# Performance work log

Hardware: AMD Instinct MI355X
Metric: run time of the kernel (lower is better)

Reference implementation:

```python
import jax, jax.numpy as jnp
import numpy as np

DIM = 1024
HEADS = 16
SCALE = DIM ** -0.5  # NOTE: original uses full dim, not head dim


def setup_inputs() -> dict:
    key = jax.random.key(0)
    k1, k2, k3, k4 = jax.random.split(key, 4)
    x = jax.random.normal(k1, (2, 2048, DIM), dtype=jnp.float32)
    # torch nn.Linear(dim, 3*dim, bias=False): y = x @ W_qkv (stored here as [dim, 3*dim])
    w_qkv = jax.random.normal(k2, (DIM, 3 * DIM), dtype=jnp.float32) * (DIM ** -0.5)
    w_out = jax.random.normal(k3, (DIM, DIM), dtype=jnp.float32) * (DIM ** -0.5)
    b_out = jax.random.normal(k4, (DIM,), dtype=jnp.float32) * 0.01
    return {"x": x, "w_qkv": w_qkv, "w_out": w_out, "b_out": b_out}


def reference(x, w_qkv, w_out, b_out):
    b, n, d = x.shape
    h = HEADS
    hd = d // h
    qkv = x @ w_qkv  # [b, n, 3*d]
    # last dim layout is (qkv, h, hd) per rearrange 'b n (qkv h d) -> qkv b h n d'
    qkv = qkv.reshape(b, n, 3, h, hd)
    q, k, v = (jnp.moveaxis(qkv, (2, 3), (0, 2))[i] for i in range(3))  # each [b, h, n, hd]
    dots = jnp.einsum('bhid,bhjd->bhij', q, k) * SCALE
    causal_mask = jnp.triu(jnp.ones((n, n), dtype=bool), k=1)
    dots = jnp.where(causal_mask, -jnp.inf, dots)
    attn = jax.nn.softmax(dots, axis=-1)
    out = jnp.einsum('bhij,bhjd->bhid', attn, v)
    out = jnp.moveaxis(out, 1, 2).reshape(b, n, d)  # 'b h n d -> b n (h d)'
    return out @ w_out + b_out
```

## Files before the change

kernel.cpp:

```cpp
#include <hip/hip_runtime.h>

typedef __attribute__((ext_vector_type(8))) short bf16x8;
typedef __attribute__((ext_vector_type(4))) float f32x4;
typedef unsigned short u16;
typedef unsigned int u32;

#define SEQ 2048
#define NHEAD 16
#define EXP2_SCALE 0.045084219f

__device__ __forceinline__ u16 f2bf(float f){
  u32 u = __builtin_bit_cast(u32, f);
  u += 0x7FFFu + ((u >> 16) & 1u);
  return (u16)(u >> 16);
}

__device__ __forceinline__ void gl16(const u16* g, u16* l){
  __builtin_amdgcn_global_load_lds(
      (__attribute__((address_space(1))) void*)(unsigned long long)(const void*)g,
      (__attribute__((address_space(3))) void*)(unsigned)(unsigned long long)(const void*)l,
      16, 0, 0);
}

__global__ __launch_bounds__(256) void prep(const float* __restrict__ x,
                                            const float* __restrict__ w_qkv,
                                            const float* __restrict__ w_out,
                                            u16* __restrict__ xb,
                                            u16* __restrict__ wqkvT,
                                            u16* __restrict__ woutT){
  __shared__ u16 t[32][33];
  const int bid = blockIdx.x;
  if (bid < 4096){
    int i = (bid * 256 + threadIdx.x) << 2;
    float4 v = *(const float4*)&x[i];
    ushort4 o;
    o.x = f2bf(v.x); o.y = f2bf(v.y); o.z = f2bf(v.z); o.w = f2bf(v.w);
    *(ushort4*)&xb[i] = o;
    return;
  }
  const float* src; u16* dst; int R, C, bx, by;
  if (bid < 7168){ int tt = bid - 4096; src = w_qkv; dst = wqkvT; R = 1024; C = 3072; bx = tt % 96; by = tt / 96; }
  else           { int tt = bid - 7168; src = w_out; dst = woutT; R = 1024; C = 1024; bx = tt % 32; by = tt / 32; }
  const int c0 = bx << 5, r0 = by << 5;
  const int tx = threadIdx.x & 31, tg = threadIdx.x >> 5;
  #pragma unroll
  for (int i = 0; i < 4; i++){
    int r = (tg << 2) + i;
    t[r][tx] = f2bf(src[(size_t)(r0 + r) * C + (c0 + tx)]);
  }
  __syncthreads();
  #pragma unroll
  for (int i = 0; i < 4; i++){
    int c = (tg << 2) + i;
    dst[(size_t)(c0 + c) * R + (r0 + tx)] = t[tx][c];
  }
}

__device__ __forceinline__ int sw32(int row, int c){
  return row * 32 + (((c ^ ((row >> 1) & 3))) << 3);
}

__global__ __launch_bounds__(256) void gemm_qkv(const u16* __restrict__ A,
                                                const u16* __restrict__ Bt,
                                                u16* __restrict__ Qo,
                                                u16* __restrict__ Ko,
                                                u16* __restrict__ Vto){
  __shared__ u16 As[128 * 32];
  __shared__ u16 Bs[128 * 32];
  const int tid = threadIdx.x;
  const int lane = tid & 63, wid = tid >> 6;
  const int l15 = lane & 15, quad = lane >> 4;
  const int wm = wid >> 1, wn = wid & 1;
  const int bm = blockIdx.y << 7, bn = blockIdx.x << 7;

  const int rT = wid * 32 + (lane >> 2);
  const int cT = (lane & 3) ^ ((rT >> 1) & 3);
  const u16* gA0 = A  + (size_t)(bm + rT) * 1024 + cT * 8;
  const u16* gB0 = Bt + (size_t)(bn + rT) * 1024 + cT * 8;
  u16* lA0 = &As[wid * 1024];
  u16* lB0 = &Bs[wid * 1024];

  f32x4 acc[4][4];
  #pragma unroll
  for (int i = 0; i < 4; i++)
    #pragma unroll
    for (int j = 0; j < 4; j++) acc[i][j] = (f32x4){0.f, 0.f, 0.f, 0.f};

  for (int k0 = 0; k0 < 1024; k0 += 32){
    gl16(gA0 + k0,            lA0);
    gl16(gA0 + k0 + 16*1024,  lA0 + 512);
    gl16(gB0 + k0,            lB0);
    gl16(gB0 + k0 + 16*1024,  lB0 + 512);
    __syncthreads();

    bf16x8 af[4], bfr[4];
    #pragma unroll
    for (int mt = 0; mt < 4; mt++)
      af[mt] = *(const bf16x8*)&As[sw32(wm * 64 + mt * 16 + l15, quad)];
    #pragma unroll
    for (int nt = 0; nt < 4; nt++)
      bfr[nt] = *(const bf16x8*)&Bs[sw32(wn * 64 + nt * 16 + l15, quad)];
    #pragma unroll
    for (int mt = 0; mt < 4; mt++)
      #pragma unroll
      for (int nt = 0; nt < 4; nt++)
        acc[mt][nt] = __builtin_amdgcn_mfma_f32_16x16x32_bf16(af[mt], bfr[nt], acc[mt][nt], 0, 0, 0);
    __syncthreads();
  }

  const int qkv_idx = bn >> 10;
  #pragma unroll
  for (int mt = 0; mt < 4; mt++){
    #pragma unroll
    for (int nt = 0; nt < 4; nt++){
      int col = bn + wn * 64 + nt * 16 + l15;
      int head = (col & 1023) >> 6, hd_i = col & 63;
      #pragma unroll
      for (int r = 0; r < 4; r++){
        int row = bm + wm * 64 + mt * 16 + quad * 4 + r;
        int b = row >> 11, pos = row & 2047;
        size_t bh = ((size_t)(b * NHEAD + head)) << 17;
        u16 v = f2bf(acc[mt][nt][r]);
        if (qkv_idx == 0)      Qo[bh + ((size_t)pos << 6) + hd_i] = v;
        else if (qkv_idx == 1) Ko[bh + ((size_t)pos << 6) + hd_i] = v;
        else                   Vto[bh + ((size_t)hd_i << 11) + pos] = v;
      }
    }
  }
}

__global__ __launch_bounds__(256) void attn_kernel(const u16* __restrict__ Q,
                                                   const u16* __restrict__ K,
                                                   const u16* __restrict__ Vt,
                                                   u16* __restrict__ Oo){
  __shared__ u16 Qs[64 * 72];
  __shared__ u16 Ks[128 * 64];
  __shared__ u16 Vts[64 * 128];
  __shared__ u16 Ps[4][16 * 136];
  const int tid = threadIdx.x;
  const int lane = tid & 63, wid = tid >> 6;
  const int l15 = lane & 15, quad = lane >> 4;
  const int bh = blockIdx.x & 31;
  const int qt = 31 - (blockIdx.x >> 5);
  const size_t base = ((size_t)bh) << 17;
  const int b = bh >> 4, h = bh & 15;

  {
    const u16* src = Q + base + ((size_t)(qt << 6) << 6);
    #pragma unroll
    for (int t = 0; t < 2; t++){
      int c = tid + (t << 8);
      int row = c >> 3, off = (c & 7) << 3;
      *(uint4*)&Qs[row * 72 + off] = *(const uint4*)&src[row * 64 + off];
    }
  }

  const int rK = wid * 32 + (lane >> 3);
  const int cK = (lane & 7) ^ (rK & 7);
  const u16* gK0 = K + base + ((size_t)rK << 6) + cK * 8;
  u16* lK = &Ks[wid * 4 * 512];
  const u16* gV[4];
  #pragma unroll
  for (int t = 0; t < 4; t++){
    int rv = wid * 16 + t * 4 + (lane >> 4);
    int cv = (lane & 15) ^ (rv & 15);
    gV[t] = Vt + base + (size_t)rv * 2048 + cv * 8;
  }
  u16* lV = &Vts[wid * 4 * 512];

  f32x4 o[4];
  #pragma unroll
  for (int dt = 0; dt < 4; dt++) o[dt] = (f32x4){0.f, 0.f, 0.f, 0.f};
  float l = 0.f;
  const int qpos = (qt << 6) + wid * 16 + l15;
  const int jt_max = qt >> 1;
  u16* Pw = &Ps[wid][0];

  for (int jt = 0; jt <= jt_max; jt++){
    const u16* gk = gK0 + (size_t)jt * 8192;
    #pragma unroll
    for (int t = 0; t < 4; t++) gl16(gk + t * 512, lK + t * 512);
    #pragma unroll
    for (int t = 0; t < 4; t++) gl16(gV[t] + (jt << 7), lV + t * 512);
    __syncthreads();

    f32x4 st[8];
    #pragma unroll
    for (int mt = 0; mt < 8; mt++) st[mt] = (f32x4){0.f, 0.f, 0.f, 0.f};
    #pragma unroll
    for (int ks = 0; ks < 2; ks++){
      bf16x8 bq = *(const bf16x8*)&Qs[(wid * 16 + l15) * 72 + ks * 32 + quad * 8];
      #pragma unroll
      for (int mt = 0; mt < 8; mt++){
        int kvr = mt * 16 + l15;
        bf16x8 ak = *(const bf16x8*)&Ks[kvr * 64 + (((ks * 4 + quad) ^ (kvr & 7)) << 3)];
        st[mt] = __builtin_amdgcn_mfma_f32_16x16x32_bf16(ak, bq, st[mt], 0, 0, 0);
      }
    }

    const bool diag = (jt == jt_max);
    float rs = 0.f;
    #pragma unroll
    for (int mt = 0; mt < 8; mt++){
      float pr[4];
      #pragma unroll
      for (int r = 0; r < 4; r++){
        float w = st[mt][r] * EXP2_SCALE;
        if (diag){
          int kv = (jt << 7) + mt * 16 + quad * 4 + r;
          if (kv > qpos) w = -INFINITY;
        }
        pr[r] = __builtin_amdgcn_exp2f(w);
      }
      rs += (pr[0] + pr[1]) + (pr[2] + pr[3]);
      u32 a0 = __builtin_bit_cast(u32, pr[0]) + 0x8000u;
      u32 a1 = __builtin_bit_cast(u32, pr[1]) + 0x8000u;
      u32 a2 = __builtin_bit_cast(u32, pr[2]) + 0x8000u;
      u32 a3 = __builtin_bit_cast(u32, pr[3]) + 0x8000u;
      uint2 pk;
      pk.x = __builtin_amdgcn_perm(a1, a0, 0x07060302u);
      pk.y = __builtin_amdgcn_perm(a3, a2, 0x07060302u);
      *(uint2*)&Pw[l15 * 136 + mt * 16 + quad * 4] = pk;
    }
    rs += __shfl_xor(rs, 16);
    rs += __shfl_xor(rs, 32);
    l += rs;

    #pragma unroll
    for (int ks = 0; ks < 4; ks++){
      bf16x8 bp = *(const bf16x8*)&Pw[l15 * 136 + ks * 32 + quad * 8];
      #pragma unroll
      for (int dt = 0; dt < 4; dt++){
        int dr = dt * 16 + l15;
        bf16x8 av = *(const bf16x8*)&Vts[dr * 128 + (((ks * 4 + quad) ^ (dr & 15)) << 3)];
        o[dt] = __builtin_amdgcn_mfma_f32_16x16x32_bf16(av, bp, o[dt], 0, 0, 0);
      }
    }
    __syncthreads();
  }

  float inv = 1.f / l;
  const size_t orow = (size_t)((b << 11) + qpos) * 1024 + h * 64;
  #pragma unroll
  for (int dt = 0; dt < 4; dt++){
    ushort4 w;
    w.x = f2bf(o[dt][0] * inv); w.y = f2bf(o[dt][1] * inv);
    w.z = f2bf(o[dt][2] * inv); w.w = f2bf(o[dt][3] * inv);
    *(ushort4*)&Oo[orow + dt * 16 + quad * 4] = w;
  }
}

__global__ __launch_bounds__(256) void gemm_out(const u16* __restrict__ A,
                                                const u16* __restrict__ Bt,
                                                const float* __restrict__ bias,
                                                float* __restrict__ out){
  __shared__ u16 As[128 * 32];
  __shared__ u16 Bs[128 * 32];
  const int tid = threadIdx.x;
  const int lane = tid & 63, wid = tid >> 6;
  const int l15 = lane & 15, quad = lane >> 4;
  const int wm = wid >> 1, wn = wid & 1;
  const int bm = blockIdx.y << 7, bn = blockIdx.x << 7;

  const int rT = wid * 32 + (lane >> 2);
  const int cT = (lane & 3) ^ ((rT >> 1) & 3);
  const u16* gA0 = A  + (size_t)(bm + rT) * 1024 + cT * 8;
  const u16* gB0 = Bt + (size_t)(bn + rT) * 1024 + cT * 8;
  u16* lA0 = &As[wid * 1024];
  u16* lB0 = &Bs[wid * 1024];

  f32x4 acc[4][4];
  #pragma unroll
  for (int i = 0; i < 4; i++)
    #pragma unroll
    for (int j = 0; j < 4; j++) acc[i][j] = (f32x4){0.f, 0.f, 0.f, 0.f};

  for (int k0 = 0; k0 < 1024; k0 += 32){
    gl16(gA0 + k0,            lA0);
    gl16(gA0 + k0 + 16*1024,  lA0 + 512);
    gl16(gB0 + k0,            lB0);
    gl16(gB0 + k0 + 16*1024,  lB0 + 512);
    __syncthreads();

    bf16x8 af[4], bfr[4];
    #pragma unroll
    for (int mt = 0; mt < 4; mt++)
      af[mt] = *(const bf16x8*)&As[sw32(wm * 64 + mt * 16 + l15, quad)];
    #pragma unroll
    for (int nt = 0; nt < 4; nt++)
      bfr[nt] = *(const bf16x8*)&Bs[sw32(wn * 64 + nt * 16 + l15, quad)];
    #pragma unroll
    for (int mt = 0; mt < 4; mt++)
      #pragma unroll
      for (int nt = 0; nt < 4; nt++)
        acc[mt][nt] = __builtin_amdgcn_mfma_f32_16x16x32_bf16(af[mt], bfr[nt], acc[mt][nt], 0, 0, 0);
    __syncthreads();
  }

  #pragma unroll
  for (int nt = 0; nt < 4; nt++){
    int col = bn + wn * 64 + nt * 16 + l15;
    float bv = bias[col];
    #pragma unroll
    for (int mt = 0; mt < 4; mt++)
      #pragma unroll
      for (int r = 0; r < 4; r++){
        int row = bm + wm * 64 + mt * 16 + quad * 4 + r;
        out[(size_t)row * 1024 + col] = acc[mt][nt][r] + bv;
      }
  }
}

extern "C" void kernel_launch(void* const* d_in, const int* in_sizes, int n_in,
                              void* d_out, int out_size, void* d_ws, size_t ws_size,
                              hipStream_t stream){
  const float* x     = (const float*)d_in[0];
  const float* w_qkv = (const float*)d_in[1];
  const float* w_out = (const float*)d_in[2];
  const float* b_out = (const float*)d_in[3];
  float* out = (float*)d_out;

  char* ws = (char*)d_ws;
  u16* xb    = (u16*)(ws);
  u16* wqkvT = (u16*)(ws + (8u  << 20));
  u16* woutT = (u16*)(ws + (14u << 20));
  u16* Qb    = (u16*)(ws + (16u << 20));
  u16* Kb    = (u16*)(ws + (24u << 20));
  u16* Vtb   = (u16*)(ws + (32u << 20));
  u16* attn  = (u16*)(ws + (40u << 20));

  prep<<<8192, 256, 0, stream>>>(x, w_qkv, w_out, xb, wqkvT, woutT);
  gemm_qkv<<<dim3(24, 32), 256, 0, stream>>>(xb, wqkvT, Qb, Kb, Vtb);
  attn_kernel<<<dim3(1024), 256, 0, stream>>>(Qb, Kb, Vtb, attn);
  gemm_out<<<dim3(8, 32), 256, 0, stream>>>(attn, woutT, b_out, out);
}
```

Baseline: 183.2 us.

## Fold softmax scale into Q, keep Q in registers, transpose V-tile MFMA

The QKV GEMM now multiplies Q by the exp2 softmax scale before rounding to bf16, so the attention kernel no longer scales each score. The attention kernel loads its Q fragments straight from global memory into registers instead of staging them through shared memory. The V-projection blocks swap the MFMA operands so each lane holds consecutive sequence positions, which makes the transposed V stores more contiguous. Pre-scaling Q before bf16 rounding changes numerics slightly, and the GEMM loop is now duplicated across two branches.

```diff
diff --git a/kernel.cpp b/kernel.cpp
--- a/kernel.cpp
+++ b/kernel.cpp
@@ -72,6 +72,7 @@
   const int l15 = lane & 15, quad = lane >> 4;
   const int wm = wid >> 1, wn = wid & 1;
   const int bm = blockIdx.y << 7, bn = blockIdx.x << 7;
+  const int qkv_idx = bn >> 10;
 
   const int rT = wid * 32 + (lane >> 2);
   const int cT = (lane & 3) ^ ((rT >> 1) & 3);
@@ -86,44 +87,79 @@
     #pragma unroll
     for (int j = 0; j < 4; j++) acc[i][j] = (f32x4){0.f, 0.f, 0.f, 0.f};
 
-  for (int k0 = 0; k0 < 1024; k0 += 32){
-    gl16(gA0 + k0,            lA0);
-    gl16(gA0 + k0 + 16*1024,  lA0 + 512);
-    gl16(gB0 + k0,            lB0);
-    gl16(gB0 + k0 + 16*1024,  lB0 + 512);
-    __syncthreads();
-
-    bf16x8 af[4], bfr[4];
-    #pragma unroll
-    for (int mt = 0; mt < 4; mt++)
-      af[mt] = *(const bf16x8*)&As[sw32(wm * 64 + mt * 16 + l15, quad)];
-    #pragma unroll
-    for (int nt = 0; nt < 4; nt++)
-      bfr[nt] = *(const bf16x8*)&Bs[sw32(wn * 64 + nt * 16 + l15, quad)];
-    #pragma unroll
-    for (int mt = 0; mt < 4; mt++)
+  if (qkv_idx != 2){
+    for (int k0 = 0; k0 < 1024; k0 += 32){
+      gl16(gA0 + k0,            lA0);
+      gl16(gA0 + k0 + 16*1024,  lA0 + 512);
+      gl16(gB0 + k0,            lB0);
+      gl16(gB0 + k0 + 16*1024,  lB0 + 512);
+      __syncthreads();
+      bf16x8 af[4], bfr[4];
+      #pragma unroll
+      for (int mt = 0; mt < 4; mt++)
+        af[mt] = *(const bf16x8*)&As[sw32(wm * 64 + mt * 16 + l15, quad)];
       #pragma unroll
       for (int nt = 0; nt < 4; nt++)
-        acc[mt][nt] = __builtin_amdgcn_mfma_f32_16x16x32_bf16(af[mt], bfr[nt], acc[mt][nt], 0, 0, 0);
-    __syncthreads();
-  }
-
-  const int qkv_idx = bn >> 10;
-  #pragma unroll
-  for (int mt = 0; mt < 4; mt++){
-    #pragma unroll
-    for (int nt = 0; nt < 4; nt++){
-      int col = bn + wn * 64 + nt * 16 + l15;
-      int head = (col & 1023) >> 6, hd_i = col & 63;
-      #pragma unroll
-      for (int r = 0; r < 4; r++){
-        int row = bm + wm * 64 + mt * 16 + quad * 4 + r;
-        int b = row >> 11, pos = row & 2047;
-        size_t bh = ((size_t)(b * NHEAD + head)) << 17;
-        u16 v = f2bf(acc[mt][nt][r]);
-        if (qkv_idx == 0)      Qo[bh + ((size_t)pos << 6) + hd_i] = v;
-        else if (qkv_idx == 1) Ko[bh + ((size_t)pos << 6) + hd_i] = v;
-        else                   Vto[bh + ((size_t)hd_i << 11) + pos] = v;
+        bfr[nt] = *(const bf16x8*)&Bs[sw32(wn * 64 + nt * 16 + l15, quad)];
+      #pragma unroll
+      for (int mt = 0; mt < 4; mt++)
+        #pragma unroll
+        for (int nt = 0; nt < 4; nt++)
+          acc[mt][nt] = __builtin_amdgcn_mfma_f32_16x16x32_bf16(af[mt], bfr[nt], acc[mt][nt], 0, 0, 0);
+      __syncthreads();
+    }
+    const float qscale = (qkv_idx == 0) ? EXP2_SCALE : 1.0f;
+    #pragma unroll
+    for (int mt = 0; mt < 4; mt++){
+      #pragma unroll
+      for (int nt = 0; nt < 4; nt++){
+        int col = bn + wn * 64 + nt * 16 + l15;
+        int head = (col & 1023) >> 6, hd_i = col & 63;
+        #pragma unroll
+        for (int r = 0; r < 4; r++){
+          int row = bm + wm * 64 + mt * 16 + quad * 4 + r;
+          int b = row >> 11, pos = row & 2047;
+          size_t bh = ((size_t)(b * NHEAD + head)) << 17;
+          u16 v = f2bf(acc[mt][nt][r] * qscale);
+          if (qkv_idx == 0) Qo[bh + ((size_t)pos << 6) + hd_i] = v;
+          else              Ko[bh + ((size_t)pos << 6) + hd_i] = v;
+        }
+      }
+    }
+  } else {
+    for (int k0 = 0; k0 < 1024; k0 += 32){
+      gl16(gA0 + k0,            lA0);
+      gl16(gA0 + k0 + 16*1024,  lA0 + 512);
+      gl16(gB0 + k0,            lB0);
+      gl16(gB0 + k0 + 16*1024,  lB0 + 512);
+      __syncthreads();
+      bf16x8 af[4], bfr[4];
+      #pragma unroll
+      for (int mt = 0; mt < 4; mt++)
+        af[mt] = *(const bf16x8*)&As[sw32(wm * 64 + mt * 16 + l15, quad)];
+      #pragma unroll
+      for (int nt = 0; nt < 4; nt++)
+        bfr[nt] = *(const bf16x8*)&Bs[sw32(wn * 64 + nt * 16 + l15, quad)];
+      #pragma unroll
+      for (int mt = 0; mt < 4; mt++)
+        #pragma unroll
+        for (int nt = 0; nt < 4; nt++)
+          acc[mt][nt] = __builtin_amdgcn_mfma_f32_16x16x32_bf16(bfr[nt], af[mt], acc[mt][nt], 0, 0, 0);
+      __syncthreads();
+    }
+    #pragma unroll
+    for (int mt = 0; mt < 4; mt++){
+      int row_m = bm + wm * 64 + mt * 16 + l15;
+      int b = row_m >> 11, pos = row_m & 2047;
+      #pragma unroll
+      for (int nt = 0; nt < 4; nt++){
+        #pragma unroll
+        for (int r = 0; r < 4; r++){
+          int c = bn + wn * 64 + nt * 16 + quad * 4 + r;
+          int head = (c & 1023) >> 6, hd_i = c & 63;
+          size_t bh = ((size_t)(b * NHEAD + head)) << 17;
+          Vto[bh + ((size_t)hd_i << 11) + pos] = f2bf(acc[mt][nt][r]);
+        }
       }
     }
   }
@@ -133,7 +169,6 @@
                                                    const u16* __restrict__ K,
                                                    const u16* __restrict__ Vt,
                                                    u16* __restrict__ Oo){
-  __shared__ u16 Qs[64 * 72];
   __shared__ u16 Ks[128 * 64];
   __shared__ u16 Vts[64 * 128];
   __shared__ u16 Ps[4][16 * 136];
@@ -145,15 +180,9 @@
   const size_t base = ((size_t)bh) << 17;
   const int b = bh >> 4, h = bh & 15;
 
-  {
-    const u16* src = Q + base + ((size_t)(qt << 6) << 6);
-    #pragma unroll
-    for (int t = 0; t < 2; t++){
-      int c = tid + (t << 8);
-      int row = c >> 3, off = (c & 7) << 3;
-      *(uint4*)&Qs[row * 72 + off] = *(const uint4*)&src[row * 64 + off];
-    }
-  }
+  const u16* qsrc = Q + base + ((size_t)((qt << 6) + wid * 16 + l15) << 6) + quad * 8;
+  const bf16x8 bq0 = *(const bf16x8*)qsrc;
+  const bf16x8 bq1 = *(const bf16x8*)(qsrc + 32);
 
   const int rK = wid * 32 + (lane >> 3);
   const int cK = (lane & 7) ^ (rK & 7);
@@ -188,14 +217,12 @@
     #pragma unroll
     for (int mt = 0; mt < 8; mt++) st[mt] = (f32x4){0.f, 0.f, 0.f, 0.f};
     #pragma unroll
-    for (int ks = 0; ks < 2; ks++){
-      bf16x8 bq = *(const bf16x8*)&Qs[(wid * 16 + l15) * 72 + ks * 32 + quad * 8];
-      #pragma unroll
-      for (int mt = 0; mt < 8; mt++){
-        int kvr = mt * 16 + l15;
-        bf16x8 ak = *(const bf16x8*)&Ks[kvr * 64 + (((ks * 4 + quad) ^ (kvr & 7)) << 3)];
-        st[mt] = __builtin_amdgcn_mfma_f32_16x16x32_bf16(ak, bq, st[mt], 0, 0, 0);
-      }
+    for (int mt = 0; mt < 8; mt++){
+      int kvr = mt * 16 + l15;
+      bf16x8 ak0 = *(const bf16x8*)&Ks[kvr * 64 + ((quad ^ (kvr & 7)) << 3)];
+      st[mt] = __builtin_amdgcn_mfma_f32_16x16x32_bf16(ak0, bq0, st[mt], 0, 0, 0);
+      bf16x8 ak1 = *(const bf16x8*)&Ks[kvr * 64 + (((4 + quad) ^ (kvr & 7)) << 3)];
+      st[mt] = __builtin_amdgcn_mfma_f32_16x16x32_bf16(ak1, bq1, st[mt], 0, 0, 0);
     }
 
     const bool diag = (jt == jt_max);
@@ -205,7 +232,7 @@
       float pr[4];
       #pragma unroll
       for (int r = 0; r < 4; r++){
-        float w = st[mt][r] * EXP2_SCALE;
+        float w = st[mt][r];
         if (diag){
           int kv = (jt << 7) + mt * 16 + quad * 4 + r;
           if (kv > qpos) w = -INFINITY;
```

Result: faster. 177.6 us (-3.0%).
